# Performance work log

Measured on AMD Instinct MI355X. Metric: run time of the kernel, lower is better.

## Reference

```python
import jax, jax.numpy as jnp
import numpy as np
from functools import partial

B, T = 2048, 500
H1, H2, D_IN, D_FC, N_CLS = 128, 64, 1, 128, 4

def _lstm_scan(x, Wih, Whh, bih, bhh, hidden, return_seq):
    # x: (B, T, D). PyTorch gate order: i, f, g, o. Weights: (4H, D) / (4H, H).
    Bsz = x.shape[0]
    b = bih + bhh
    xg = jnp.einsum('btd,gd->btg', x, Wih) + b  # precompute input projections (B,T,4H)
    xg = jnp.swapaxes(xg, 0, 1)                 # (T,B,4H)
    h0 = jnp.zeros((Bsz, hidden), x.dtype)
    c0 = jnp.zeros((Bsz, hidden), x.dtype)

    def step(carry, gt):
        h, c = carry
        gates = gt + h @ Whh.T
        i, f, g, o = jnp.split(gates, 4, axis=-1)
        c = jax.nn.sigmoid(f) * c + jax.nn.sigmoid(i) * jnp.tanh(g)
        h = jax.nn.sigmoid(o) * jnp.tanh(c)
        return (h, c), (h if return_seq else None)

    (hT, _), hs = jax.lax.scan(step, (h0, c0), xg)
    if return_seq:
        return jnp.swapaxes(hs, 0, 1)  # (B,T,H)
    return hT  # (B,H)

def setup_inputs() -> dict:
    key = jax.random.key(0)
    ks = jax.random.split(key, 16)
    n = lambda k, shape: jax.random.normal(k, shape, dtype=jnp.float32) * 0.05
    return {
        'x': jax.random.normal(ks[0], (B, 1, T), dtype=jnp.float32),
        'Wp': n(ks[1], (H1, D_IN)), 'bp': n(ks[2], (H1,)),
        'Wih1': n(ks[3], (4 * H1, H1)), 'Whh1': n(ks[4], (4 * H1, H1)),
        'bih1': n(ks[5], (4 * H1,)), 'bhh1': n(ks[6], (4 * H1,)),
        'Wih2': n(ks[7], (4 * H2, H1)), 'Whh2': n(ks[8], (4 * H2, H2)),
        'bih2': n(ks[9], (4 * H2,)), 'bhh2': n(ks[10], (4 * H2,)),
        'W1': n(ks[11], (D_FC, H2)), 'b1': n(ks[12], (D_FC,)),
        'W2': n(ks[13], (N_CLS, D_FC)), 'b2': n(ks[14], (N_CLS,)),
    }

def reference(x, Wp, bp, Wih1, Whh1, bih1, bhh1, Wih2, Whh2, bih2, bhh2, W1, b1, W2, b2):
    # x: (B,1,T) -> (B,T,1)
    h = jnp.swapaxes(x, 1, 2)
    h = h @ Wp.T + bp                                         # (B,T,128)
    h = _lstm_scan(h, Wih1, Whh1, bih1, bhh1, H1, True)       # (B,T,128); dropout is identity in eval
    h = _lstm_scan(h, Wih2, Whh2, bih2, bhh2, H2, False)      # (B,64) == last-timestep output
    h = jax.nn.relu(h @ W1.T + b1)                            # (B,128)
    return h @ W2.T + b2                                      # (B,4)
```

## Files before the change

kernel.cpp:

```cpp
#include <hip/hip_runtime.h>


#define B_   2048
#define T_   500
#define BM   8
#define NBLK (B_ / BM)
#define NTHR 768

typedef __attribute__((ext_vector_type(8))) short bf16x8;
typedef __attribute__((ext_vector_type(4))) float f32x4;

#define LOG2E 1.44269504088896340736f

static __device__ __forceinline__ short f2bf(float f) {
  unsigned u = __builtin_bit_cast(unsigned, f);
  u = (u + 0x7fffu + ((u >> 16) & 1u)) >> 16;
  return (short)u;
}

static __device__ __forceinline__ float lstm_cell_s(float gi, float gf, float gg,
                                                    float go, float& c) {
  float Ei = __builtin_amdgcn_exp2f(-gi);
  float Eg = __builtin_amdgcn_exp2f(gg + gg);
  float Ef = __builtin_amdgcn_exp2f(-gf);
  float Eo = __builtin_amdgcn_exp2f(-go);
  float t12 = (1.f + Ei) * (1.f + Eg);
  float num = c * t12 + (Eg - 1.f) * (1.f + Ef);
  c = num * __builtin_amdgcn_rcpf((1.f + Ef) * t12);
  float Ec = __builtin_amdgcn_exp2f(2.88539008177792681472f * c);
  return (Ec - 1.f) * __builtin_amdgcn_rcpf((1.f + Eo) * (1.f + Ec));
}

__global__ __launch_bounds__(NTHR)
void lstm_fused(const float* __restrict__ X,
                const float* __restrict__ Wp,
                const float* __restrict__ bp,
                const float* __restrict__ Wih1,
                const float* __restrict__ Whh1,
                const float* __restrict__ bih1,
                const float* __restrict__ bhh1,
                const float* __restrict__ Wih2,
                const float* __restrict__ Whh2,
                const float* __restrict__ bih2,
                const float* __restrict__ bhh2,
                const float* __restrict__ W1,
                const float* __restrict__ b1,
                const float* __restrict__ W2,
                const float* __restrict__ b2,
                float* __restrict__ Out) {
  __shared__ __align__(16) short h1b[2][16][136];
  __shared__ __align__(16) short h2b[2][16][72];
  __shared__ __align__(16) float xs[T_][16];
  __shared__ float h2f[8][64];
  __shared__ float fc1s[8][132];

  const int tid = threadIdx.x;
  const int ln = tid & 63;
  const int wv = tid >> 6;
  const int cl = ln & 15;
  const int kg = ln >> 4;
  const int r0 = blockIdx.x * BM;
  const bool isL1 = (wv >= 4);
  const int w1 = wv - 4;

  bf16x8 Wreg[4][4];
  bf16x8 W2h[4][2];
  float uv[8];

  if (isL1) {
#pragma unroll
    for (int n = 0; n < 4; ++n) {
      const int R = n * 128 + 16 * w1 + cl;
      float u = 0.f, vv = bih1[R] + bhh1[R];
      const float4* Wi4 = (const float4*)(Wih1 + R * 128);
      const float4* Wp4 = (const float4*)Wp;
      const float4* bp4 = (const float4*)bp;
#pragma unroll 4
      for (int d = 0; d < 32; ++d) {
        float4 a = Wi4[d], pw = Wp4[d], qb = bp4[d];
        u  += a.x*pw.x + a.y*pw.y + a.z*pw.z + a.w*pw.w;
        vv += a.x*qb.x + a.y*qb.y + a.z*qb.z + a.w*qb.w;
      }
      uv[n] = u * LOG2E;
      uv[4 + n] = vv * LOG2E;
#pragma unroll
      for (int kf = 0; kf < 4; ++kf) {
        const float4* s4 = (const float4*)(Whh1 + R * 128 + kf * 32 + kg * 8);
        float4 a0 = s4[0], a1 = s4[1];
        bf16x8 fr;
        fr[0]=f2bf(a0.x*LOG2E); fr[1]=f2bf(a0.y*LOG2E);
        fr[2]=f2bf(a0.z*LOG2E); fr[3]=f2bf(a0.w*LOG2E);
        fr[4]=f2bf(a1.x*LOG2E); fr[5]=f2bf(a1.y*LOG2E);
        fr[6]=f2bf(a1.z*LOG2E); fr[7]=f2bf(a1.w*LOG2E);
        Wreg[n][kf] = fr;
      }
    }
  } else {
#pragma unroll
    for (int n = 0; n < 4; ++n) {
      const int R = n * 64 + 16 * wv + cl;
      uv[n] = (bih2[R] + bhh2[R]) * LOG2E;
#pragma unroll
      for (int kf = 0; kf < 4; ++kf) {
        const float4* s4 = (const float4*)(Wih2 + R * 128 + kf * 32 + kg * 8);
        float4 a0 = s4[0], a1 = s4[1];
        bf16x8 fr;
        fr[0]=f2bf(a0.x*LOG2E); fr[1]=f2bf(a0.y*LOG2E);
        fr[2]=f2bf(a0.z*LOG2E); fr[3]=f2bf(a0.w*LOG2E);
        fr[4]=f2bf(a1.x*LOG2E); fr[5]=f2bf(a1.y*LOG2E);
        fr[6]=f2bf(a1.z*LOG2E); fr[7]=f2bf(a1.w*LOG2E);
        Wreg[n][kf] = fr;
      }
#pragma unroll
      for (int kf = 0; kf < 2; ++kf) {
        const float4* s4 = (const float4*)(Whh2 + R * 64 + kf * 32 + kg * 8);
        float4 a0 = s4[0], a1 = s4[1];
        bf16x8 fr;
        fr[0]=f2bf(a0.x*LOG2E); fr[1]=f2bf(a0.y*LOG2E);
        fr[2]=f2bf(a0.z*LOG2E); fr[3]=f2bf(a0.w*LOG2E);
        fr[4]=f2bf(a1.x*LOG2E); fr[5]=f2bf(a1.y*LOG2E);
        fr[6]=f2bf(a1.z*LOG2E); fr[7]=f2bf(a1.w*LOG2E);
        W2h[n][kf] = fr;
      }
    }
  }

  for (int i = tid; i < 2 * 16 * 136; i += NTHR) ((short*)h1b)[i] = 0;
  for (int i = tid; i < 2 * 16 * 72;  i += NTHR) ((short*)h2b)[i] = 0;
  for (int i = tid; i < T_ * 16; i += NTHR) ((float*)xs)[i] = 0.f;
  __syncthreads();
#pragma unroll
  for (int r = 0; r < 8; ++r)
    for (int t = tid; t < T_; t += NTHR)
      xs[t][r] = X[(size_t)(r0 + r) * T_ + t];
  __syncthreads();

  float c0 = 0.f, c1 = 0.f;
  const int rA = (kg < 2) ? kg * 4 : (kg - 2) * 4 + 2;
  const int rB = rA + 1;
  const int uu = 16 * (isL1 ? w1 : wv) + cl;

#define L1_STEP(i, cur, prv)                                                  \
  {                                                                           \
    bf16x8 a1[4];                                                             \
    _Pragma("unroll")                                                         \
    for (int kf = 0; kf < 4; ++kf)                                            \
      a1[kf] = *(const bf16x8*)&h1b[prv][cl][kf * 32 + kg * 8];               \
    f32x4 xr4 = *(const f32x4*)&xs[i][kg * 4];                                \
    f32x4 acc[4];                                                             \
    _Pragma("unroll")                                                         \
    for (int n = 0; n < 4; ++n) {                                             \
      _Pragma("unroll")                                                       \
      for (int e = 0; e < 4; ++e)                                             \
        acc[n][e] = xr4[e] * uv[n] + uv[4 + n];                               \
    }                                                                         \
    __builtin_amdgcn_s_setprio(1);                                            \
    _Pragma("unroll")                                                         \
    for (int n = 0; n < 4; ++n)                                               \
      _Pragma("unroll")                                                       \
      for (int kf = 0; kf < 4; ++kf)                                          \
        acc[n] = __builtin_amdgcn_mfma_f32_16x16x32_bf16(                     \
            a1[kf], Wreg[n][kf], acc[n], 0, 0, 0);                            \
    __builtin_amdgcn_s_setprio(0);                                            \
    float gA[4], gB[4];                                                       \
    _Pragma("unroll")                                                         \
    for (int n = 0; n < 4; ++n) {                                             \
      float s2 = __shfl_xor(acc[n][2], 32);                                   \
      float s3 = __shfl_xor(acc[n][3], 32);                                   \
      gA[n] = (kg < 2) ? acc[n][0] : s2;                                      \
      gB[n] = (kg < 2) ? acc[n][1] : s3;                                      \
    }                                                                         \
    float hA = lstm_cell_s(gA[0], gA[1], gA[2], gA[3], c0);                   \
    float hB = lstm_cell_s(gB[0], gB[1], gB[2], gB[3], c1);                   \
    unsigned pk;                                                              \
    asm("v_cvt_pk_bf16_f32 %0, %1, %2" : "=v"(pk) : "v"(hA), "v"(hB));        \
    h1b[cur][rA][uu] = (short)pk;                                             \
    h1b[cur][rB][uu] = (short)(pk >> 16);                                     \
  }

#define L2_STEP(cur, prv, FINAL)                                              \
  {                                                                           \
    bf16x8 a1[4], ag[2];                                                      \
    _Pragma("unroll")                                                         \
    for (int kf = 0; kf < 4; ++kf)                                            \
      a1[kf] = *(const bf16x8*)&h1b[prv][cl][kf * 32 + kg * 8];               \
    _Pragma("unroll")                                                         \
    for (int kf = 0; kf < 2; ++kf)                                            \
      ag[kf] = *(const bf16x8*)&h2b[cur][cl][kf * 32 + kg * 8];               \
    f32x4 acc[4];                                                             \
    _Pragma("unroll")                                                         \
    for (int n = 0; n < 4; ++n)                                               \
      acc[n] = (f32x4){uv[n], uv[n], uv[n], uv[n]};                           \
    __builtin_amdgcn_s_setprio(1);                                            \
    _Pragma("unroll")                                                         \
    for (int n = 0; n < 4; ++n) {                                             \
      acc[n] = __builtin_amdgcn_mfma_f32_16x16x32_bf16(ag[0], W2h[n][0],      \
                                                       acc[n], 0, 0, 0);      \
      acc[n] = __builtin_amdgcn_mfma_f32_16x16x32_bf16(ag[1], W2h[n][1],      \
                                                       acc[n], 0, 0, 0);      \
      _Pragma("unroll")                                                       \
      for (int kf = 0; kf < 4; ++kf)                                          \
        acc[n] = __builtin_amdgcn_mfma_f32_16x16x32_bf16(                     \
            a1[kf], Wreg[n][kf], acc[n], 0, 0, 0);                            \
    }                                                                         \
    __builtin_amdgcn_s_setprio(0);                                            \
    float gA[4], gB[4];                                                       \
    _Pragma("unroll")                                                         \
    for (int n = 0; n < 4; ++n) {                                             \
      float s2 = __shfl_xor(acc[n][2], 32);                                   \
      float s3 = __shfl_xor(acc[n][3], 32);                                   \
      gA[n] = (kg < 2) ? acc[n][0] : s2;                                      \
      gB[n] = (kg < 2) ? acc[n][1] : s3;                                      \
    }                                                                         \
    float hA = lstm_cell_s(gA[0], gA[1], gA[2], gA[3], c0);                   \
    float hB = lstm_cell_s(gB[0], gB[1], gB[2], gB[3], c1);                   \
    unsigned pk;                                                              \
    asm("v_cvt_pk_bf16_f32 %0, %1, %2" : "=v"(pk) : "v"(hA), "v"(hB));        \
    h2b[prv][rA][uu] = (short)pk;                                             \
    h2b[prv][rB][uu] = (short)(pk >> 16);                                     \
    if (FINAL) { h2f[rA][uu] = hA; h2f[rB][uu] = hB; }                        \
  }

  if (isL1) L1_STEP(0, 0, 1);
  __syncthreads();

  for (int i = 1; i < T_; ++i) {
    const int cur = i & 1, prv = cur ^ 1;
    if (isL1) {
      L1_STEP(i, cur, prv);
    } else {
      L2_STEP(cur, prv, 0);
    }
    __syncthreads();
  }

  if (!isL1) L2_STEP(0, 1, 1);
  __syncthreads();

  if (tid < 512) {
    const int u = tid & 127, r2 = tid >> 7;
    float a0 = b1[u], a1f = b1[u];
    for (int k = 0; k < 64; ++k) {
      float w = W1[u * 64 + k];
      a0  += h2f[r2 * 2 + 0][k] * w;
      a1f += h2f[r2 * 2 + 1][k] * w;
    }
    fc1s[r2 * 2 + 0][u] = fmaxf(a0, 0.f);
    fc1s[r2 * 2 + 1][u] = fmaxf(a1f, 0.f);
  }
  __syncthreads();
  if (tid < 32) {
    const int r = tid >> 2, cls = tid & 3;
    float a = b2[cls];
    for (int k = 0; k < 128; ++k) a += fc1s[r][k] * W2[cls * 128 + k];
    Out[(size_t)(r0 + r) * 4 + cls] = a;
  }
}

extern "C" void kernel_launch(void* const* d_in, const int* in_sizes, int n_in,
                              void* d_out, int out_size, void* d_ws, size_t ws_size,
                              hipStream_t stream) {
  const float* X    = (const float*)d_in[0];
  const float* Wp   = (const float*)d_in[1];
  const float* bp   = (const float*)d_in[2];
  const float* Wih1 = (const float*)d_in[3];
  const float* Whh1 = (const float*)d_in[4];
  const float* bih1 = (const float*)d_in[5];
  const float* bhh1 = (const float*)d_in[6];
  const float* Wih2 = (const float*)d_in[7];
  const float* Whh2 = (const float*)d_in[8];
  const float* bih2 = (const float*)d_in[9];
  const float* bhh2 = (const float*)d_in[10];
  const float* W1   = (const float*)d_in[11];
  const float* b1   = (const float*)d_in[12];
  const float* W2   = (const float*)d_in[13];
  const float* b2   = (const float*)d_in[14];
  float* Out = (float*)d_out;

  hipLaunchKernelGGL(lstm_fused, dim3(NBLK), dim3(NTHR), 0, stream,
                     X, Wp, bp, Wih1, Whh1, bih1, bhh1,
                     Wih2, Whh2, bih2, bhh2, W1, b1, W2, b2, Out);
}
```

Measured before the change: 553.2 us.

## Store hidden states in MFMA fragment layout and move layer-2 recurrent weights to LDS

Hidden-state buffers for both layers are reorganised into per-lane MFMA operand fragments, so each lane reads a contiguous 16-byte fragment instead of a strided row slice. The input sequence buffer is compacted to 8 rows per timestep, with a mask zeroing the rows that do not belong to the lane. Layer-2 recurrent weights move from registers into shared memory to relieve register pressure, at the cost of extra LDS reads on every step. The FC1 scratch buffer reuses the input buffer to save shared memory.

```diff
diff --git a/kernel.cpp b/kernel.cpp
--- a/kernel.cpp
+++ b/kernel.cpp
@@ -48,11 +48,11 @@
                 const float* __restrict__ W2,
                 const float* __restrict__ b2,
                 float* __restrict__ Out) {
-  __shared__ __align__(16) short h1b[2][16][136];
-  __shared__ __align__(16) short h2b[2][16][72];
-  __shared__ __align__(16) float xs[T_][16];
+  __shared__ __align__(16) short h1f[2][4][64][8];
+  __shared__ __align__(16) short h2g[2][2][64][8];
+  __shared__ __align__(16) short w2h[4][4][2][64][8];
+  __shared__ __align__(16) float xsb[T_ * 8];
   __shared__ float h2f[8][64];
-  __shared__ float fc1s[8][132];
 
   const int tid = threadIdx.x;
   const int ln = tid & 63;
@@ -64,7 +64,6 @@
   const int w1 = wv - 4;
 
   bf16x8 Wreg[4][4];
-  bf16x8 W2h[4][2];
   float uv[8];
 
   if (isL1) {
@@ -115,38 +114,39 @@
       for (int kf = 0; kf < 2; ++kf) {
         const float4* s4 = (const float4*)(Whh2 + R * 64 + kf * 32 + kg * 8);
         float4 a0 = s4[0], a1 = s4[1];
-        bf16x8 fr;
-        fr[0]=f2bf(a0.x*LOG2E); fr[1]=f2bf(a0.y*LOG2E);
-        fr[2]=f2bf(a0.z*LOG2E); fr[3]=f2bf(a0.w*LOG2E);
-        fr[4]=f2bf(a1.x*LOG2E); fr[5]=f2bf(a1.y*LOG2E);
-        fr[6]=f2bf(a1.z*LOG2E); fr[7]=f2bf(a1.w*LOG2E);
-        W2h[n][kf] = fr;
-      }
-    }
-  }
-
-  for (int i = tid; i < 2 * 16 * 136; i += NTHR) ((short*)h1b)[i] = 0;
-  for (int i = tid; i < 2 * 16 * 72;  i += NTHR) ((short*)h2b)[i] = 0;
-  for (int i = tid; i < T_ * 16; i += NTHR) ((float*)xs)[i] = 0.f;
-  __syncthreads();
+        short* dst = &w2h[wv][n][kf][ln][0];
+        dst[0]=f2bf(a0.x*LOG2E); dst[1]=f2bf(a0.y*LOG2E);
+        dst[2]=f2bf(a0.z*LOG2E); dst[3]=f2bf(a0.w*LOG2E);
+        dst[4]=f2bf(a1.x*LOG2E); dst[5]=f2bf(a1.y*LOG2E);
+        dst[6]=f2bf(a1.z*LOG2E); dst[7]=f2bf(a1.w*LOG2E);
+      }
+    }
+  }
+
+  for (int i = tid; i < 2 * 4 * 64 * 8; i += NTHR) ((short*)h1f)[i] = 0;
+  for (int i = tid; i < 2 * 2 * 64 * 8; i += NTHR) ((short*)h2g)[i] = 0;
 #pragma unroll
   for (int r = 0; r < 8; ++r)
     for (int t = tid; t < T_; t += NTHR)
-      xs[t][r] = X[(size_t)(r0 + r) * T_ + t];
+      xsb[t * 8 + r] = X[(size_t)(r0 + r) * T_ + t];
   __syncthreads();
 
   float c0 = 0.f, c1 = 0.f;
   const int rA = (kg < 2) ? kg * 4 : (kg - 2) * 4 + 2;
   const int rB = rA + 1;
   const int uu = 16 * (isL1 ? w1 : wv) + cl;
+  const int wkf = uu >> 5, wg = ((uu >> 3) & 3) * 16, wel = uu & 7;
+  const float xmask = (kg < 2) ? 1.f : 0.f;
 
 #define L1_STEP(i, cur, prv)                                                  \
   {                                                                           \
     bf16x8 a1[4];                                                             \
     _Pragma("unroll")                                                         \
     for (int kf = 0; kf < 4; ++kf)                                            \
-      a1[kf] = *(const bf16x8*)&h1b[prv][cl][kf * 32 + kg * 8];               \
-    f32x4 xr4 = *(const f32x4*)&xs[i][kg * 4];                                \
+      a1[kf] = *(const bf16x8*)&h1f[prv][kf][ln][0];                          \
+    f32x4 xr4 = *(const f32x4*)&xsb[(i) * 8 + (kg & 1) * 4];                  \
+    _Pragma("unroll")                                                         \
+    for (int e = 0; e < 4; ++e) xr4[e] *= xmask;                              \
     f32x4 acc[4];                                                             \
     _Pragma("unroll")                                                         \
     for (int n = 0; n < 4; ++n) {                                             \
@@ -174,8 +174,8 @@
     float hB = lstm_cell_s(gB[0], gB[1], gB[2], gB[3], c1);                   \
     unsigned pk;                                                              \
     asm("v_cvt_pk_bf16_f32 %0, %1, %2" : "=v"(pk) : "v"(hA), "v"(hB));        \
-    h1b[cur][rA][uu] = (short)pk;                                             \
-    h1b[cur][rB][uu] = (short)(pk >> 16);                                     \
+    h1f[cur][wkf][wg + rA][wel] = (short)pk;                                  \
+    h1f[cur][wkf][wg + rB][wel] = (short)(pk >> 16);                          \
   }
 
 #define L2_STEP(cur, prv, FINAL)                                              \
@@ -183,10 +183,10 @@
     bf16x8 a1[4], ag[2];                                                      \
     _Pragma("unroll")                                                         \
     for (int kf = 0; kf < 4; ++kf)                                            \
-      a1[kf] = *(const bf16x8*)&h1b[prv][cl][kf * 32 + kg * 8];               \
+      a1[kf] = *(const bf16x8*)&h1f[prv][kf][ln][0];                          \
     _Pragma("unroll")                                                         \
     for (int kf = 0; kf < 2; ++kf)                                            \
-      ag[kf] = *(const bf16x8*)&h2b[cur][cl][kf * 32 + kg * 8];               \
+      ag[kf] = *(const bf16x8*)&h2g[cur][kf][ln][0];                          \
     f32x4 acc[4];                                                             \
     _Pragma("unroll")                                                         \
     for (int n = 0; n < 4; ++n)                                               \
@@ -194,9 +194,11 @@
     __builtin_amdgcn_s_setprio(1);                                            \
     _Pragma("unroll")                                                         \
     for (int n = 0; n < 4; ++n) {                                             \
-      acc[n] = __builtin_amdgcn_mfma_f32_16x16x32_bf16(ag[0], W2h[n][0],      \
+      bf16x8 w0 = *(const bf16x8*)&w2h[wv][n][0][ln][0];                      \
+      bf16x8 w1f = *(const bf16x8*)&w2h[wv][n][1][ln][0];                     \
+      acc[n] = __builtin_amdgcn_mfma_f32_16x16x32_bf16(ag[0], w0,             \
                                                        acc[n], 0, 0, 0);      \
-      acc[n] = __builtin_amdgcn_mfma_f32_16x16x32_bf16(ag[1], W2h[n][1],      \
+      acc[n] = __builtin_amdgcn_mfma_f32_16x16x32_bf16(ag[1], w1f,            \
                                                        acc[n], 0, 0, 0);      \
       _Pragma("unroll")                                                       \
       for (int kf = 0; kf < 4; ++kf)                                          \
@@ -216,8 +218,8 @@
     float hB = lstm_cell_s(gB[0], gB[1], gB[2], gB[3], c1);                   \
     unsigned pk;                                                              \
     asm("v_cvt_pk_bf16_f32 %0, %1, %2" : "=v"(pk) : "v"(hA), "v"(hB));        \
-    h2b[prv][rA][uu] = (short)pk;                                             \
-    h2b[prv][rB][uu] = (short)(pk >> 16);                                     \
+    h2g[prv][wkf][wg + rA][wel] = (short)pk;                                  \
+    h2g[prv][wkf][wg + rB][wel] = (short)(pk >> 16);                          \
     if (FINAL) { h2f[rA][uu] = hA; h2f[rB][uu] = hB; }                        \
   }
 
@@ -237,6 +239,7 @@
   if (!isL1) L2_STEP(0, 1, 1);
   __syncthreads();
 
+  float* fc1s = xsb;
   if (tid < 512) {
     const int u = tid & 127, r2 = tid >> 7;
     float a0 = b1[u], a1f = b1[u];
@@ -245,14 +248,14 @@
       a0  += h2f[r2 * 2 + 0][k] * w;
       a1f += h2f[r2 * 2 + 1][k] * w;
     }
-    fc1s[r2 * 2 + 0][u] = fmaxf(a0, 0.f);
-    fc1s[r2 * 2 + 1][u] = fmaxf(a1f, 0.f);
+    fc1s[(r2 * 2 + 0) * 132 + u] = fmaxf(a0, 0.f);
+    fc1s[(r2 * 2 + 1) * 132 + u] = fmaxf(a1f, 0.f);
   }
   __syncthreads();
   if (tid < 32) {
     const int r = tid >> 2, cls = tid & 3;
     float a = b2[cls];
-    for (int k = 0; k < 128; ++k) a += fc1s[r][k] * W2[cls * 128 + k];
+    for (int k = 0; k < 128; ++k) a += fc1s[r * 132 + k] * W2[cls * 128 + k];
     Out[(size_t)(r0 + r) * 4 + cls] = a;
   }
 }
```

Measured after the change: 511.4 us. 7.6% less time.
